# Performance work log

Measured on AMD Instinct MI355X. Metric: run time of the kernel, lower is better.

The kernel has to match this reference:

```python
import jax, jax.numpy as jnp
import numpy as np

B, T, E, U, V = 64, 100, 512, 512, 32000


def gru_layer(xs_tm, Wg, bg, Wc, bc):
    """TF GRUCell math. xs_tm: [T, B, D]. Returns (ys [T,B,U], h_final [B,U])."""
    u_dim = Wc.shape[1]
    h0 = jnp.zeros((xs_tm.shape[1], u_dim), xs_tm.dtype)

    def step(h, x):
        ru = jax.nn.sigmoid(jnp.concatenate([x, h], -1) @ Wg + bg)
        r, u = jnp.split(ru, 2, axis=-1)
        c = jnp.tanh(jnp.concatenate([x, r * h], -1) @ Wc + bc)
        h_new = u * h + (1.0 - u) * c
        return h_new, h_new

    h_final, ys = jax.lax.scan(step, h0, xs_tm)
    return ys, h_final


def setup_inputs() -> dict:
    key = jax.random.key(0)
    ks = jax.random.split(key, 16)

    def w(k, shape):
        fan_in = shape[0]
        return jax.random.normal(k, shape, jnp.float32) * (1.0 / np.sqrt(fan_in))

    inp = {
        "x": jax.random.randint(ks[0], (B, T), 0, V, jnp.int32),
        "embedding": jax.random.normal(ks[1], (V, E), jnp.float32) * 0.02,
        # bi-directional layer, input dim E
        "Wg_fw": w(ks[2], (E + U, 2 * U)), "bg_fw": jnp.ones((2 * U,), jnp.float32),
        "Wc_fw": w(ks[3], (E + U, U)),     "bc_fw": jnp.zeros((U,), jnp.float32),
        "Wg_bw": w(ks[4], (E + U, 2 * U)), "bg_bw": jnp.ones((2 * U,), jnp.float32),
        "Wc_bw": w(ks[5], (E + U, U)),     "bc_bw": jnp.zeros((U,), jnp.float32),
        # uni layer 1, input dim 2U (concat fw/bw)
        "Wg_u1": w(ks[6], (2 * U + U, 2 * U)), "bg_u1": jnp.ones((2 * U,), jnp.float32),
        "Wc_u1": w(ks[7], (2 * U + U, U)),     "bc_u1": jnp.zeros((U,), jnp.float32),
        # uni layer 2, input dim U
        "Wg_u2": w(ks[8], (U + U, 2 * U)), "bg_u2": jnp.ones((2 * U,), jnp.float32),
        "Wc_u2": w(ks[9], (U + U, U)),     "bc_u2": jnp.zeros((U,), jnp.float32),
    }
    return inp


def reference(x, embedding, Wg_fw, bg_fw, Wc_fw, bc_fw, Wg_bw, bg_bw, Wc_bw, bc_bw,
              Wg_u1, bg_u1, Wc_u1, bc_u1, Wg_u2, bg_u2, Wc_u2, bc_u2):
    emb = embedding[x]                      # [B, T, E] embedding lookup
    xs = jnp.swapaxes(emb, 0, 1)            # [T, B, E] time-major for scan
    # bidirectional GRU layer
    yf, _ = gru_layer(xs, Wg_fw, bg_fw, Wc_fw, bc_fw)
    yb, _ = gru_layer(xs[::-1], Wg_bw, bg_bw, Wc_bw, bc_bw)
    a = jnp.concatenate([yf, yb[::-1]], -1)  # [T, B, 2U]
    # 2-layer unidirectional GRU stack (MultiRNNCell)
    a, s1 = gru_layer(a, Wg_u1, bg_u1, Wc_u1, bc_u1)
    a, s2 = gru_layer(a, Wg_u2, bg_u2, Wc_u2, bc_u2)
    output = jnp.swapaxes(a, 0, 1)          # [B, T, U]
    state = jnp.stack([s1, s2])             # [2, B, U] per-layer final states
    return output, state
```

## Files before the change

### kernel.cpp

```cpp
#include <hip/hip_runtime.h>
#include <hip/hip_bf16.h>


#define TT 100

using f32x4 = __attribute__((ext_vector_type(4))) float;
using s16x8 = __attribute__((ext_vector_type(8))) short;

__device__ __forceinline__ unsigned short f2bfu(float x) {
  __hip_bfloat16 b = __float2bfloat16(x);
  unsigned short u;
  __builtin_memcpy(&u, &b, sizeof(u));
  return u;
}
__device__ __forceinline__ float bfu2f(unsigned short u) {
  __hip_bfloat16 b;
  __builtin_memcpy(&b, &u, sizeof(b));
  return __bfloat162float(b);
}
__device__ __forceinline__ float sigm(float x) {
  x = fminf(fmaxf(x, -30.f), 30.f);
  return 1.f / (1.f + __expf(-x));
}
__device__ __forceinline__ float tanh_fast(float x) {
  x = fminf(fmaxf(x, -15.f), 15.f);
  float e = __expf(-2.f * x);
  return (1.f - e) / (1.f + e);
}

__device__ __forceinline__ s16x8 sc1_load_b128(const void* p) {
  s16x8 v;
  asm volatile("global_load_dwordx4 %0, %1, off sc0 sc1" : "=v"(v) : "v"(p) : "memory");
  return v;
}
__device__ __forceinline__ void sc1_store_b16(void* p, unsigned v) {
  asm volatile("global_store_short %0, %1, off sc0 sc1" :: "v"(p), "v"(v) : "memory");
}
__device__ __forceinline__ void vm_drain() {
  asm volatile("s_waitcnt vmcnt(0)" ::: "memory");
}

__global__ __launch_bounds__(256) void pack_w_kernel(const float* __restrict__ Wg,
                                                     const float* __restrict__ Wc,
                                                     int ldg, int ldc, int ktTot,
                                                     unsigned short* __restrict__ hi,
                                                     unsigned short* __restrict__ lo) {
  const int gg = blockIdx.x * 256 + threadIdx.x;
  if (gg >= 96 * ktTot * 64) return;
  const int lane = gg & 63;
  const int pair = gg >> 6;
  const int kt = pair % ktTot;
  const int nt = pair / ktTot;
  const int kg = lane >> 4;
  const int nl = lane & 15;
  const size_t off = (size_t)gg * 8;
  for (int i = 0; i < 8; ++i) {
    const int k = kt * 32 + kg * 8 + i;
    float v = (nt < 64) ? Wg[(size_t)k * ldg + nt * 16 + nl]
                        : Wc[(size_t)k * ldc + (nt - 64) * 16 + nl];
    unsigned short h = f2bfu(v);
    hi[off + i] = h;
    lo[off + i] = f2bfu(v - bfu2f(h));
  }
}

template <int ASRC>
__global__ __launch_bounds__(256) void gemm_mfma(
    const int* __restrict__ xtok, const float* __restrict__ emb,
    const unsigned short* __restrict__ aHi, const unsigned short* __restrict__ aLo, int lda,
    const unsigned short* __restrict__ bHi, const unsigned short* __restrict__ bLo,
    int ktTot, int ktX,
    const float* __restrict__ bg, const float* __restrict__ bc,
    float* __restrict__ C) {
  __shared__ unsigned short Ah[128 * 40];
  __shared__ unsigned short Al[128 * 40];

  const int tid = threadIdx.x;
  const int lane = tid & 63;
  const int w = tid >> 6;
  const int bm = blockIdx.x, bn = blockIdx.y;
  const int fm = lane & 15, fkg = lane >> 4;

  const int arow = tid >> 1;
  const int koff = (tid & 1) * 16;
  const int rowg = bm * 128 + arow;
  int embIdx = 0;
  if (ASRC == 0) {
    const int t_ = rowg >> 6, b_ = rowg & 63;
    embIdx = xtok[b_ * TT + t_];
  }

  f32x4 acc[2][8];
#pragma unroll
  for (int rt = 0; rt < 2; ++rt)
#pragma unroll
    for (int ni = 0; ni < 8; ++ni) acc[rt][ni] = (f32x4){0.f, 0.f, 0.f, 0.f};

  for (int kt = 0; kt < ktX; ++kt) {
    __syncthreads();
    if (ASRC == 0) {
      const float* src = emb + (size_t)embIdx * 512 + kt * 32 + koff;
      s16x8 h0, h1, l0, l1;
#pragma unroll
      for (int c = 0; c < 2; ++c) {
        f32x4 va = *(const f32x4*)(src + c * 8);
        f32x4 vb = *(const f32x4*)(src + c * 8 + 4);
        s16x8 hh, ll;
#pragma unroll
        for (int j = 0; j < 4; ++j) {
          unsigned short h = f2bfu(va[j]);
          hh[j] = (short)h; ll[j] = (short)f2bfu(va[j] - bfu2f(h));
          unsigned short h2 = f2bfu(vb[j]);
          hh[j + 4] = (short)h2; ll[j + 4] = (short)f2bfu(vb[j] - bfu2f(h2));
        }
        if (c == 0) { h0 = hh; l0 = ll; } else { h1 = hh; l1 = ll; }
      }
      *(s16x8*)(Ah + arow * 40 + koff) = h0;
      *(s16x8*)(Ah + arow * 40 + koff + 8) = h1;
      *(s16x8*)(Al + arow * 40 + koff) = l0;
      *(s16x8*)(Al + arow * 40 + koff + 8) = l1;
    } else {
      const size_t so = (size_t)rowg * lda + kt * 32 + koff;
      s16x8 h0 = *(const s16x8*)(aHi + so);
      s16x8 h1 = *(const s16x8*)(aHi + so + 8);
      s16x8 l0 = *(const s16x8*)(aLo + so);
      s16x8 l1 = *(const s16x8*)(aLo + so + 8);
      *(s16x8*)(Ah + arow * 40 + koff) = h0;
      *(s16x8*)(Ah + arow * 40 + koff + 8) = h1;
      *(s16x8*)(Al + arow * 40 + koff) = l0;
      *(s16x8*)(Al + arow * 40 + koff + 8) = l1;
    }
    __syncthreads();

    s16x8 ah[2], al[2];
#pragma unroll
    for (int rt = 0; rt < 2; ++rt) {
      const int m = w * 32 + rt * 16 + fm;
      ah[rt] = *(const s16x8*)(Ah + m * 40 + fkg * 8);
      al[rt] = *(const s16x8*)(Al + m * 40 + fkg * 8);
    }
#pragma unroll
    for (int ni = 0; ni < 8; ++ni) {
      const int nt = bn * 8 + ni;
      const size_t bo = ((size_t)nt * ktTot + kt) * 512 + lane * 8;
      s16x8 bh = *(const s16x8*)(bHi + bo);
      s16x8 bl = *(const s16x8*)(bLo + bo);
#pragma unroll
      for (int rt = 0; rt < 2; ++rt) {
        acc[rt][ni] = __builtin_amdgcn_mfma_f32_16x16x32_bf16(ah[rt], bh, acc[rt][ni], 0, 0, 0);
        acc[rt][ni] = __builtin_amdgcn_mfma_f32_16x16x32_bf16(ah[rt], bl, acc[rt][ni], 0, 0, 0);
        acc[rt][ni] = __builtin_amdgcn_mfma_f32_16x16x32_bf16(al[rt], bh, acc[rt][ni], 0, 0, 0);
      }
    }
  }

#pragma unroll
  for (int ni = 0; ni < 8; ++ni) {
    const int nt = bn * 8 + ni;
    int dcol; float bias;
    if (nt < 64) { dcol = nt * 16 + fm; bias = bg[dcol]; }
    else { dcol = 1024 + (nt - 64) * 16 + fm; bias = bc[(nt - 64) * 16 + fm]; }
#pragma unroll
    for (int rt = 0; rt < 2; ++rt)
#pragma unroll
      for (int j = 0; j < 4; ++j) {
        const int row = bm * 128 + w * 32 + rt * 16 + fkg * 4 + j;
        C[(size_t)row * 1536 + dcol] = acc[rt][ni][j] + bias;
      }
  }
}

template <int NB>
__global__ __launch_bounds__(256, 1) void gru_scan_kernel(
    const float* __restrict__ gxF, const float* __restrict__ gxB,
    const unsigned short* __restrict__ wHiF, const unsigned short* __restrict__ wLoF,
    const unsigned short* __restrict__ wHiB, const unsigned short* __restrict__ wLoB,
    int ktTot, int ktH0,
    unsigned short* __restrict__ hHiG, unsigned short* __restrict__ hLoG,
    unsigned short* __restrict__ rHiG, unsigned short* __restrict__ rLoG,
    unsigned* __restrict__ slots,
    unsigned short* __restrict__ yHi, unsigned short* __restrict__ yLo, int yld,
    float* __restrict__ outb,
    float* __restrict__ stout) {
  __shared__ unsigned short wHi_s[3 * 8192];
  __shared__ unsigned short wLo_s[3 * 8192];
  __shared__ unsigned short hHi_s[8192];
  __shared__ unsigned short hLo_s[8192];
  __shared__ float scr[4][16][17];
  __shared__ float scr2[4][16][17];

  const int tid = threadIdx.x;
  const int lane = tid & 63;
  const int wv = tid >> 6;
  const int bid = blockIdx.x;
  const int g = bid & 7;
  const int wg = bid >> 3;
  const int hs = wg << 4;

  int dir = 0, b0;
  const float* gx;
  const unsigned short *wph, *wpl;
  if (NB == 16) {
    dir = g & 1;
    b0 = (g >> 1) << 4;
    gx = dir ? gxB : gxF;
    wph = dir ? wHiB : wHiF;
    wpl = dir ? wLoB : wLoF;
  } else {
    b0 = g * NB;
    gx = gxF;
    wph = wHiF;
    wpl = wLoF;
  }

  {
    const int nt0[3] = {wg, 32 + wg, 64 + wg};
    for (int c = 0; c < 3; ++c) {
      const unsigned short* sH = wph + ((size_t)nt0[c] * ktTot + ktH0) * 512;
      const unsigned short* sL = wpl + ((size_t)nt0[c] * ktTot + ktH0) * 512;
      unsigned short* dH = wHi_s + c * 8192;
      unsigned short* dL = wLo_s + c * 8192;
#pragma unroll
      for (int it = 0; it < 4; ++it) {
        const int o = (it * 256 + tid) * 8;
        *(s16x8*)(dH + o) = *(const s16x8*)(sH + o);
        *(s16x8*)(dL + o) = *(const s16x8*)(sL + o);
      }
    }
  }
  {
    s16x8 z = {0, 0, 0, 0, 0, 0, 0, 0};
#pragma unroll
    for (int it = 0; it < 4; ++it) {
      const int o = (it * 256 + tid) * 8;
      *(s16x8*)(hHi_s + o) = z;
      *(s16x8*)(hLo_s + o) = z;
    }
  }
  __syncthreads();

  unsigned* gslots = slots + g * 32;

  const int fm = lane & 15;
  const int fkg = lane >> 4;
  const int arow = fm * 512;
  const int asw = (fm & 7) << 3;
  const int akof = fkg * 8;

  const int ob = tid >> 4, oj = tid & 15;
  const bool own = (ob < NB);
  const int ui = ob * 512 + ((hs + oj) ^ ((ob & 7) << 3));

  const size_t tileo = (size_t)g * 8192;

  auto mfma_tile = [&](int cidx, float (*dst)[16][17]) {
    f32x4 acc0 = {0.f, 0.f, 0.f, 0.f}, acc1 = {0.f, 0.f, 0.f, 0.f};
    const int ktb = wv * 4;
#pragma unroll
    for (int q = 0; q < 4; ++q) {
      const int kt = ktb + q;
      const int ao = arow + ((kt * 32 + akof) ^ asw);
      s16x8 ah = *(const s16x8*)(hHi_s + ao);
      s16x8 al = *(const s16x8*)(hLo_s + ao);
      const int wo = ((cidx * 16 + kt) * 64 + lane) * 8;
      s16x8 bh = *(const s16x8*)(wHi_s + wo);
      s16x8 bl = *(const s16x8*)(wLo_s + wo);
      if (q & 1) {
        acc1 = __builtin_amdgcn_mfma_f32_16x16x32_bf16(ah, bh, acc1, 0, 0, 0);
        acc1 = __builtin_amdgcn_mfma_f32_16x16x32_bf16(ah, bl, acc1, 0, 0, 0);
        acc1 = __builtin_amdgcn_mfma_f32_16x16x32_bf16(al, bh, acc1, 0, 0, 0);
      } else {
        acc0 = __builtin_amdgcn_mfma_f32_16x16x32_bf16(ah, bh, acc0, 0, 0, 0);
        acc0 = __builtin_amdgcn_mfma_f32_16x16x32_bf16(ah, bl, acc0, 0, 0, 0);
        acc0 = __builtin_amdgcn_mfma_f32_16x16x32_bf16(al, bh, acc0, 0, 0, 0);
      }
    }
#pragma unroll
    for (int j = 0; j < 4; ++j) dst[wv][fkg * 4 + j][fm] = acc0[j] + acc1[j];
  };

  auto load_tile = [&](const unsigned short* SH, const unsigned short* SL) {
    s16x8 th[NB / 4], tl[NB / 4];
#pragma unroll
    for (int it = 0; it < NB / 4; ++it) {
      const int o = (it * 256 + tid) * 8;
      th[it] = sc1_load_b128(SH + tileo + o);
      tl[it] = sc1_load_b128(SL + tileo + o);
    }
    vm_drain();
#pragma unroll
    for (int it = 0; it < NB / 4; ++it) {
      const int o = (it * 256 + tid) * 8;
      *(s16x8*)(hHi_s + o) = th[it];
      *(s16x8*)(hLo_s + o) = tl[it];
    }
  };

  auto poll = [&](unsigned target) {
    if (tid < 32) {
      const unsigned* p = gslots + tid;
      unsigned v;
      do {
        asm volatile("global_load_dword %0, %1, off sc0 sc1\n\ts_waitcnt vmcnt(0)"
                     : "=v"(v) : "v"(p) : "memory");
      } while (!__all(v >= target));
    }
    __syncthreads();
  };

  float gxr = 0.f, gxu = 0.f, gxc = 0.f;
  if (own) {
    const float* row = gx + ((size_t)(dir ? TT - 1 : 0) * 64 + b0 + ob) * 1536 + hs + oj;
    gxr = row[0]; gxu = row[512]; gxc = row[1024];
  }

  for (int t = 0; t < TT; ++t) {
    const int tg = dir ? (TT - 1 - t) : t;

    mfma_tile(0, scr);
    __syncthreads();

    float hv = 0.f;
    if (own) {
      float rpre = scr[0][ob][oj] + scr[1][ob][oj] + scr[2][ob][oj] + scr[3][ob][oj] + gxr;
      float sg = sigm(rpre);
      hv = bfu2f(hHi_s[ui]) + bfu2f(hLo_s[ui]);
      float rh = sg * hv;
      unsigned short rhh = f2bfu(rh);
      sc1_store_b16(rHiG + tileo + ui, rhh);
      sc1_store_b16(rLoG + tileo + ui, f2bfu(rh - bfu2f(rhh)));
    }
    vm_drain();
    __syncthreads();
    if (tid == 0) {
      unsigned* p = gslots + wg;
      unsigned tv = 2 * t + 1;
      asm volatile("global_store_dword %0, %1, off sc0 sc1" :: "v"(p), "v"(tv) : "memory");
    }

    mfma_tile(1, scr2);

    float ngxr = 0.f, ngxu = 0.f, ngxc = 0.f;
    if (own && t + 1 < TT) {
      const int tgn = dir ? (TT - 2 - t) : (t + 1);
      const float* row = gx + ((size_t)tgn * 64 + b0 + ob) * 1536 + hs + oj;
      ngxr = row[0]; ngxu = row[512]; ngxc = row[1024];
    }

    poll(2 * t + 1);
    load_tile(rHiG, rLoG);
    __syncthreads();

    mfma_tile(2, scr);
    __syncthreads();

    float hn = 0.f;
    unsigned short hh_ = 0, ll_ = 0;
    if (own) {
      float upre = scr2[0][ob][oj] + scr2[1][ob][oj] + scr2[2][ob][oj] + scr2[3][ob][oj] + gxu;
      float uv = sigm(upre);
      float cpre = scr[0][ob][oj] + scr[1][ob][oj] + scr[2][ob][oj] + scr[3][ob][oj] + gxc;
      float cv = tanh_fast(cpre);
      hn = uv * hv + (1.f - uv) * cv;
      hh_ = f2bfu(hn);
      ll_ = f2bfu(hn - bfu2f(hh_));
    }

    if (t == TT - 1) {
      if (own) {
        if (yHi) {
          const int ycol = (NB == 16) ? (dir * 512 + hs + oj) : (hs + oj);
          const size_t yi = ((size_t)tg * 64 + (b0 + ob)) * yld + ycol;
          yHi[yi] = hh_; yLo[yi] = ll_;
        }
        if (outb) outb[((size_t)(b0 + ob) * TT + t) * 512 + hs + oj] = hn;
        if (stout) stout[(size_t)(b0 + ob) * 512 + hs + oj] = hn;
      }
      break;
    }

    if (own) {
      sc1_store_b16(hHiG + tileo + ui, hh_);
      sc1_store_b16(hLoG + tileo + ui, ll_);
    }
    vm_drain();
    __syncthreads();
    if (tid == 0) {
      unsigned* p = gslots + wg;
      unsigned tv = 2 * t + 2;
      asm volatile("global_store_dword %0, %1, off sc0 sc1" :: "v"(p), "v"(tv) : "memory");
    }

    if (own) {
      if (yHi) {
        const int ycol = (NB == 16) ? (dir * 512 + hs + oj) : (hs + oj);
        const size_t yi = ((size_t)tg * 64 + (b0 + ob)) * yld + ycol;
        yHi[yi] = hh_; yLo[yi] = ll_;
      }
      if (outb) outb[((size_t)(b0 + ob) * TT + t) * 512 + hs + oj] = hn;
    }
    gxr = ngxr; gxu = ngxu; gxc = ngxc;

    poll(2 * t + 2);
    load_tile(hHiG, hLoG);
    __syncthreads();
  }
}

extern "C" void kernel_launch(void* const* d_in, const int* in_sizes, int n_in,
                              void* d_out, int out_size, void* d_ws, size_t ws_size,
                              hipStream_t stream) {
  (void)in_sizes; (void)n_in; (void)out_size; (void)ws_size;
  const int* x = (const int*)d_in[0];
  const float* emb = (const float*)d_in[1];
  const float* WgFw = (const float*)d_in[2];
  const float* bgFw = (const float*)d_in[3];
  const float* WcFw = (const float*)d_in[4];
  const float* bcFw = (const float*)d_in[5];
  const float* WgBw = (const float*)d_in[6];
  const float* bgBw = (const float*)d_in[7];
  const float* WcBw = (const float*)d_in[8];
  const float* bcBw = (const float*)d_in[9];
  const float* WgU1 = (const float*)d_in[10];
  const float* bgU1 = (const float*)d_in[11];
  const float* WcU1 = (const float*)d_in[12];
  const float* bcU1 = (const float*)d_in[13];
  const float* WgU2 = (const float*)d_in[14];
  const float* bgU2 = (const float*)d_in[15];
  const float* WcU2 = (const float*)d_in[16];
  const float* bcU2 = (const float*)d_in[17];

  char* ws = (char*)d_ws;
  float* bufA = (float*)(ws + 0);
  float* bufB = (float*)(ws + 39321600);
  unsigned short* ycatHi = (unsigned short*)(ws + 78643200);
  unsigned short* ycatLo = (unsigned short*)(ws + 91750400);
  unsigned short* y1Hi = (unsigned short*)(ws + 78643200);
  unsigned short* y1Lo = (unsigned short*)(ws + 85196800);
  unsigned short* wpFwHi = (unsigned short*)(ws + 104857600);
  unsigned short* wpFwLo = (unsigned short*)(ws + 108003328);
  unsigned short* wpBwHi = (unsigned short*)(ws + 111149056);
  unsigned short* wpBwLo = (unsigned short*)(ws + 114294784);
  unsigned short* wpU1Hi = (unsigned short*)(ws + 117440512);
  unsigned short* wpU1Lo = (unsigned short*)(ws + 122159104);
  unsigned short* wpU2Hi = (unsigned short*)(ws + 117440512);
  unsigned short* wpU2Lo = (unsigned short*)(ws + 120586240);
  unsigned short* hb = (unsigned short*)(ws + 126877696);
  unsigned* bars = (unsigned*)(ws + 127401984);

  unsigned short* hHiG = hb;
  unsigned short* hLoG = hb + 65536;
  unsigned short* rHiG = hb + 131072;
  unsigned short* rLoG = hb + 196608;

  float* out = (float*)d_out;
  float* st1 = out + (size_t)64 * TT * 512;
  float* st2 = st1 + 64 * 512;

  hipMemsetAsync(bars, 0, 4096, stream);

  pack_w_kernel<<<768, 256, 0, stream>>>(WgFw, WcFw, 1024, 512, 32, wpFwHi, wpFwLo);
  pack_w_kernel<<<768, 256, 0, stream>>>(WgBw, WcBw, 1024, 512, 32, wpBwHi, wpBwLo);
  pack_w_kernel<<<1152, 256, 0, stream>>>(WgU1, WcU1, 1024, 512, 48, wpU1Hi, wpU1Lo);

  gemm_mfma<0><<<dim3(50, 12), 256, 0, stream>>>(
      x, emb, nullptr, nullptr, 0, wpFwHi, wpFwLo, 32, 16, bgFw, bcFw, bufA);
  gemm_mfma<0><<<dim3(50, 12), 256, 0, stream>>>(
      x, emb, nullptr, nullptr, 0, wpBwHi, wpBwLo, 32, 16, bgBw, bcBw, bufB);

  {
    const float *a0 = bufA, *a1 = bufB;
    const unsigned short *w0 = wpFwHi, *w1 = wpFwLo, *w2 = wpBwHi, *w3 = wpBwLo;
    int ktT = 32, ktH = 16;
    unsigned short *h0 = hHiG, *h1 = hLoG, *r0 = rHiG, *r1 = rLoG;
    unsigned* bp = bars;
    unsigned short *yh = ycatHi, *yl = ycatLo; int yld = 1024;
    float *on = nullptr, *sn = nullptr;
    void* args[] = {&a0, &a1, &w0, &w1, &w2, &w3, &ktT, &ktH, &h0, &h1, &r0, &r1,
                    &bp, &yh, &yl, &yld, &on, &sn};
    hipLaunchCooperativeKernel((const void*)gru_scan_kernel<16>, dim3(256), dim3(256),
                               args, 0, stream);
  }

  gemm_mfma<1><<<dim3(50, 12), 256, 0, stream>>>(
      nullptr, nullptr, ycatHi, ycatLo, 1024, wpU1Hi, wpU1Lo, 48, 32, bgU1, bcU1, bufA);

  {
    const float *a0 = bufA, *a1 = nullptr;
    const unsigned short *w0 = wpU1Hi, *w1 = wpU1Lo, *w2 = nullptr, *w3 = nullptr;
    int ktT = 48, ktH = 32;
    unsigned short *h0 = hHiG, *h1 = hLoG, *r0 = rHiG, *r1 = rLoG;
    unsigned* bp = bars + 256;
    unsigned short *yh = y1Hi, *yl = y1Lo; int yld = 512;
    float *on = nullptr, *sn = st1;
    void* args[] = {&a0, &a1, &w0, &w1, &w2, &w3, &ktT, &ktH, &h0, &h1, &r0, &r1,
                    &bp, &yh, &yl, &yld, &on, &sn};
    hipLaunchCooperativeKernel((const void*)gru_scan_kernel<8>, dim3(256), dim3(256),
                               args, 0, stream);
  }

  pack_w_kernel<<<768, 256, 0, stream>>>(WgU2, WcU2, 1024, 512, 32, wpU2Hi, wpU2Lo);

  gemm_mfma<1><<<dim3(50, 12), 256, 0, stream>>>(
      nullptr, nullptr, y1Hi, y1Lo, 512, wpU2Hi, wpU2Lo, 32, 16, bgU2, bcU2, bufB);

  {
    const float *a0 = bufB, *a1 = nullptr;
    const unsigned short *w0 = wpU2Hi, *w1 = wpU2Lo, *w2 = nullptr, *w3 = nullptr;
    int ktT = 32, ktH = 16;
    unsigned short *h0 = hHiG, *h1 = hLoG, *r0 = rHiG, *r1 = rLoG;
    unsigned* bp = bars + 512;
    unsigned short *yh = nullptr, *yl = nullptr; int yld = 0;
    float *on = out, *sn = st2;
    void* args[] = {&a0, &a1, &w0, &w1, &w2, &w3, &ktT, &ktH, &h0, &h1, &r0, &r1,
                    &bp, &yh, &yl, &yld, &on, &sn};
    hipLaunchCooperativeKernel((const void*)gru_scan_kernel<8>, dim3(256), dim3(256),
                               args, 0, stream);
  }
}
```

Baseline: 1.783 ms.

## Load packed hidden-state fragments straight from global into registers, skipping LDS staging

The hi/lo bf16 halves of the shared hidden and reset-gated state now live interleaved in one 32-bit word in global memory. Each wave loads its MFMA A-fragments directly from global (bypassing cache) into registers and unpacks them with bit operations, instead of copying the whole tile into shared memory and paying an extra barrier. The per-step h fragments are loaded once and reused for both gate and candidate matmuls, and the global state buffer is zeroed with a memset before each scan. This is meant to cut LDS round-trips and a __syncthreads per half-step on the serial recurrence path. The cost is more global load traffic per wave and some ALU work to unpack.

```diff
diff --git a/kernel.cpp b/kernel.cpp
--- a/kernel.cpp
+++ b/kernel.cpp
@@ -6,6 +6,7 @@
 
 using f32x4 = __attribute__((ext_vector_type(4))) float;
 using s16x8 = __attribute__((ext_vector_type(8))) short;
+using u32x4 = __attribute__((ext_vector_type(4))) unsigned;
 
 __device__ __forceinline__ unsigned short f2bfu(float x) {
   __hip_bfloat16 b = __float2bfloat16(x);
@@ -26,15 +27,6 @@
   x = fminf(fmaxf(x, -15.f), 15.f);
   float e = __expf(-2.f * x);
   return (1.f - e) / (1.f + e);
-}
-
-__device__ __forceinline__ s16x8 sc1_load_b128(const void* p) {
-  s16x8 v;
-  asm volatile("global_load_dwordx4 %0, %1, off sc0 sc1" : "=v"(v) : "v"(p) : "memory");
-  return v;
-}
-__device__ __forceinline__ void sc1_store_b16(void* p, unsigned v) {
-  asm volatile("global_store_short %0, %1, off sc0 sc1" :: "v"(p), "v"(v) : "memory");
 }
 __device__ __forceinline__ void vm_drain() {
   asm volatile("s_waitcnt vmcnt(0)" ::: "memory");
@@ -176,16 +168,13 @@
     const unsigned short* __restrict__ wHiF, const unsigned short* __restrict__ wLoF,
     const unsigned short* __restrict__ wHiB, const unsigned short* __restrict__ wLoB,
     int ktTot, int ktH0,
-    unsigned short* __restrict__ hHiG, unsigned short* __restrict__ hLoG,
-    unsigned short* __restrict__ rHiG, unsigned short* __restrict__ rLoG,
+    unsigned* __restrict__ hPkG, unsigned* __restrict__ rPkG,
     unsigned* __restrict__ slots,
     unsigned short* __restrict__ yHi, unsigned short* __restrict__ yLo, int yld,
     float* __restrict__ outb,
     float* __restrict__ stout) {
   __shared__ unsigned short wHi_s[3 * 8192];
   __shared__ unsigned short wLo_s[3 * 8192];
-  __shared__ unsigned short hHi_s[8192];
-  __shared__ unsigned short hLo_s[8192];
   __shared__ float scr[4][16][17];
   __shared__ float scr2[4][16][17];
 
@@ -228,24 +217,14 @@
       }
     }
   }
-  {
-    s16x8 z = {0, 0, 0, 0, 0, 0, 0, 0};
-#pragma unroll
-    for (int it = 0; it < 4; ++it) {
-      const int o = (it * 256 + tid) * 8;
-      *(s16x8*)(hHi_s + o) = z;
-      *(s16x8*)(hLo_s + o) = z;
-    }
-  }
   __syncthreads();
 
   unsigned* gslots = slots + g * 32;
 
   const int fm = lane & 15;
   const int fkg = lane >> 4;
-  const int arow = fm * 512;
+  const int afe = fm * 512;
   const int asw = (fm & 7) << 3;
-  const int akof = fkg * 8;
 
   const int ob = tid >> 4, oj = tid & 15;
   const bool own = (ob < NB);
@@ -253,46 +232,59 @@
 
   const size_t tileo = (size_t)g * 8192;
 
-  auto mfma_tile = [&](int cidx, float (*dst)[16][17]) {
+  auto mfma_regs = [&](int cidx, const s16x8* ah, const s16x8* al,
+                       float (*dst)[16][17]) {
     f32x4 acc0 = {0.f, 0.f, 0.f, 0.f}, acc1 = {0.f, 0.f, 0.f, 0.f};
-    const int ktb = wv * 4;
 #pragma unroll
     for (int q = 0; q < 4; ++q) {
-      const int kt = ktb + q;
-      const int ao = arow + ((kt * 32 + akof) ^ asw);
-      s16x8 ah = *(const s16x8*)(hHi_s + ao);
-      s16x8 al = *(const s16x8*)(hLo_s + ao);
+      const int kt = wv * 4 + q;
       const int wo = ((cidx * 16 + kt) * 64 + lane) * 8;
       s16x8 bh = *(const s16x8*)(wHi_s + wo);
       s16x8 bl = *(const s16x8*)(wLo_s + wo);
       if (q & 1) {
-        acc1 = __builtin_amdgcn_mfma_f32_16x16x32_bf16(ah, bh, acc1, 0, 0, 0);
-        acc1 = __builtin_amdgcn_mfma_f32_16x16x32_bf16(ah, bl, acc1, 0, 0, 0);
-        acc1 = __builtin_amdgcn_mfma_f32_16x16x32_bf16(al, bh, acc1, 0, 0, 0);
+        acc1 = __builtin_amdgcn_mfma_f32_16x16x32_bf16(ah[q], bh, acc1, 0, 0, 0);
+        acc1 = __builtin_amdgcn_mfma_f32_16x16x32_bf16(ah[q], bl, acc1, 0, 0, 0);
+        acc1 = __builtin_amdgcn_mfma_f32_16x16x32_bf16(al[q], bh, acc1, 0, 0, 0);
       } else {
-        acc0 = __builtin_amdgcn_mfma_f32_16x16x32_bf16(ah, bh, acc0, 0, 0, 0);
-        acc0 = __builtin_amdgcn_mfma_f32_16x16x32_bf16(ah, bl, acc0, 0, 0, 0);
-        acc0 = __builtin_amdgcn_mfma_f32_16x16x32_bf16(al, bh, acc0, 0, 0, 0);
+        acc0 = __builtin_amdgcn_mfma_f32_16x16x32_bf16(ah[q], bh, acc0, 0, 0, 0);
+        acc0 = __builtin_amdgcn_mfma_f32_16x16x32_bf16(ah[q], bl, acc0, 0, 0, 0);
+        acc0 = __builtin_amdgcn_mfma_f32_16x16x32_bf16(al[q], bh, acc0, 0, 0, 0);
       }
     }
 #pragma unroll
     for (int j = 0; j < 4; ++j) dst[wv][fkg * 4 + j][fm] = acc0[j] + acc1[j];
   };
 
-  auto load_tile = [&](const unsigned short* SH, const unsigned short* SL) {
-    s16x8 th[NB / 4], tl[NB / 4];
-#pragma unroll
-    for (int it = 0; it < NB / 4; ++it) {
-      const int o = (it * 256 + tid) * 8;
-      th[it] = sc1_load_b128(SH + tileo + o);
-      tl[it] = sc1_load_b128(SL + tileo + o);
-    }
+  auto load_frags = [&](const unsigned* pk, s16x8* ah, s16x8* al,
+                        bool withHv, unsigned* hvOut) {
+    u32x4 d[4][2];
+#pragma unroll
+    for (int q = 0; q < 4; ++q) {
+      const int kt = wv * 4 + q;
+      const unsigned* p = pk + tileo + afe + ((kt * 32 + fkg * 8) ^ asw);
+      asm volatile("global_load_dwordx4 %0, %1, off sc0 sc1"
+                   : "=v"(d[q][0]) : "v"(p) : "memory");
+      asm volatile("global_load_dwordx4 %0, %1, off sc0 sc1"
+                   : "=v"(d[q][1]) : "v"(p + 4) : "memory");
+    }
+    if (withHv && own)
+      asm volatile("global_load_dword %0, %1, off sc0 sc1"
+                   : "=v"(*hvOut) : "v"(pk + tileo + ui) : "memory");
     vm_drain();
-#pragma unroll
-    for (int it = 0; it < NB / 4; ++it) {
-      const int o = (it * 256 + tid) * 8;
-      *(s16x8*)(hHi_s + o) = th[it];
-      *(s16x8*)(hLo_s + o) = tl[it];
+    __builtin_amdgcn_sched_barrier(0);
+#pragma unroll
+    for (int q = 0; q < 4; ++q) {
+      u32x4 hh, ll;
+#pragma unroll
+      for (int i = 0; i < 2; ++i) {
+        const u32x4 dd = d[q][i];
+        hh[2 * i] = (dd[0] & 0xffffu) | (dd[1] << 16);
+        hh[2 * i + 1] = (dd[2] & 0xffffu) | (dd[3] << 16);
+        ll[2 * i] = (dd[0] >> 16) | (dd[1] & 0xffff0000u);
+        ll[2 * i + 1] = (dd[2] >> 16) | (dd[3] & 0xffff0000u);
+      }
+      __builtin_memcpy(&ah[q], &hh, 16);
+      __builtin_memcpy(&al[q], &ll, 16);
     }
   };
 
@@ -317,28 +309,33 @@
   for (int t = 0; t < TT; ++t) {
     const int tg = dir ? (TT - 1 - t) : t;
 
-    mfma_tile(0, scr);
+    s16x8 ah[4], al[4];
+    unsigned hvu = 0;
+    load_frags(hPkG, ah, al, true, &hvu);
+    mfma_regs(0, ah, al, scr);
     __syncthreads();
 
     float hv = 0.f;
     if (own) {
       float rpre = scr[0][ob][oj] + scr[1][ob][oj] + scr[2][ob][oj] + scr[3][ob][oj] + gxr;
       float sg = sigm(rpre);
-      hv = bfu2f(hHi_s[ui]) + bfu2f(hLo_s[ui]);
+      hv = bfu2f((unsigned short)(hvu & 0xffffu)) + bfu2f((unsigned short)(hvu >> 16));
       float rh = sg * hv;
-      unsigned short rhh = f2bfu(rh);
-      sc1_store_b16(rHiG + tileo + ui, rhh);
-      sc1_store_b16(rLoG + tileo + ui, f2bfu(rh - bfu2f(rhh)));
+      unsigned short hh_ = f2bfu(rh);
+      unsigned short ll_ = f2bfu(rh - bfu2f(hh_));
+      unsigned e = (unsigned)hh_ | ((unsigned)ll_ << 16);
+      asm volatile("global_store_dword %0, %1, off sc0 sc1"
+                   :: "v"(rPkG + tileo + ui), "v"(e) : "memory");
     }
     vm_drain();
     __syncthreads();
     if (tid == 0) {
-      unsigned* p = gslots + wg;
       unsigned tv = 2 * t + 1;
-      asm volatile("global_store_dword %0, %1, off sc0 sc1" :: "v"(p), "v"(tv) : "memory");
-    }
-
-    mfma_tile(1, scr2);
+      asm volatile("global_store_dword %0, %1, off sc0 sc1"
+                   :: "v"(gslots + wg), "v"(tv) : "memory");
+    }
+
+    mfma_regs(1, ah, al, scr2);
 
     float ngxr = 0.f, ngxu = 0.f, ngxc = 0.f;
     if (own && t + 1 < TT) {
@@ -348,10 +345,9 @@
     }
 
     poll(2 * t + 1);
-    load_tile(rHiG, rLoG);
-    __syncthreads();
-
-    mfma_tile(2, scr);
+
+    load_frags(rPkG, ah, al, false, nullptr);
+    mfma_regs(2, ah, al, scr);
     __syncthreads();
 
     float hn = 0.f;
@@ -380,15 +376,16 @@
     }
 
     if (own) {
-      sc1_store_b16(hHiG + tileo + ui, hh_);
-      sc1_store_b16(hLoG + tileo + ui, ll_);
+      unsigned e = (unsigned)hh_ | ((unsigned)ll_ << 16);
+      asm volatile("global_store_dword %0, %1, off sc0 sc1"
+                   :: "v"(hPkG + tileo + ui), "v"(e) : "memory");
     }
     vm_drain();
     __syncthreads();
     if (tid == 0) {
-      unsigned* p = gslots + wg;
       unsigned tv = 2 * t + 2;
-      asm volatile("global_store_dword %0, %1, off sc0 sc1" :: "v"(p), "v"(tv) : "memory");
+      asm volatile("global_store_dword %0, %1, off sc0 sc1"
+                   :: "v"(gslots + wg), "v"(tv) : "memory");
     }
 
     if (own) {
@@ -402,8 +399,6 @@
     gxr = ngxr; gxu = ngxu; gxc = ngxc;
 
     poll(2 * t + 2);
-    load_tile(hHiG, hLoG);
-    __syncthreads();
   }
 }
 
@@ -445,13 +440,9 @@
   unsigned short* wpU1Lo = (unsigned short*)(ws + 122159104);
   unsigned short* wpU2Hi = (unsigned short*)(ws + 117440512);
   unsigned short* wpU2Lo = (unsigned short*)(ws + 120586240);
-  unsigned short* hb = (unsigned short*)(ws + 126877696);
+  unsigned* hPkG = (unsigned*)(ws + 126877696);
+  unsigned* rPkG = (unsigned*)(ws + 127139840);
   unsigned* bars = (unsigned*)(ws + 127401984);
-
-  unsigned short* hHiG = hb;
-  unsigned short* hLoG = hb + 65536;
-  unsigned short* rHiG = hb + 131072;
-  unsigned short* rLoG = hb + 196608;
 
   float* out = (float*)d_out;
   float* st1 = out + (size_t)64 * TT * 512;
@@ -468,15 +459,16 @@
   gemm_mfma<0><<<dim3(50, 12), 256, 0, stream>>>(
       x, emb, nullptr, nullptr, 0, wpBwHi, wpBwLo, 32, 16, bgBw, bcBw, bufB);
 
+  hipMemsetAsync(hPkG, 0, 524288, stream);
   {
     const float *a0 = bufA, *a1 = bufB;
     const unsigned short *w0 = wpFwHi, *w1 = wpFwLo, *w2 = wpBwHi, *w3 = wpBwLo;
     int ktT = 32, ktH = 16;
-    unsigned short *h0 = hHiG, *h1 = hLoG, *r0 = rHiG, *r1 = rLoG;
+    unsigned *h0 = hPkG, *r0 = rPkG;
     unsigned* bp = bars;
     unsigned short *yh = ycatHi, *yl = ycatLo; int yld = 1024;
     float *on = nullptr, *sn = nullptr;
-    void* args[] = {&a0, &a1, &w0, &w1, &w2, &w3, &ktT, &ktH, &h0, &h1, &r0, &r1,
+    void* args[] = {&a0, &a1, &w0, &w1, &w2, &w3, &ktT, &ktH, &h0, &r0,
                     &bp, &yh, &yl, &yld, &on, &sn};
     hipLaunchCooperativeKernel((const void*)gru_scan_kernel<16>, dim3(256), dim3(256),
                                args, 0, stream);
@@ -485,15 +477,16 @@
   gemm_mfma<1><<<dim3(50, 12), 256, 0, stream>>>(
       nullptr, nullptr, ycatHi, ycatLo, 1024, wpU1Hi, wpU1Lo, 48, 32, bgU1, bcU1, bufA);
 
+  hipMemsetAsync(hPkG, 0, 524288, stream);
   {
     const float *a0 = bufA, *a1 = nullptr;
     const unsigned short *w0 = wpU1Hi, *w1 = wpU1Lo, *w2 = nullptr, *w3 = nullptr;
     int ktT = 48, ktH = 32;
-    unsigned short *h0 = hHiG, *h1 = hLoG, *r0 = rHiG, *r1 = rLoG;
+    unsigned *h0 = hPkG, *r0 = rPkG;
     unsigned* bp = bars + 256;
     unsigned short *yh = y1Hi, *yl = y1Lo; int yld = 512;
     float *on = nullptr, *sn = st1;
-    void* args[] = {&a0, &a1, &w0, &w1, &w2, &w3, &ktT, &ktH, &h0, &h1, &r0, &r1,
+    void* args[] = {&a0, &a1, &w0, &w1, &w2, &w3, &ktT, &ktH, &h0, &r0,
                     &bp, &yh, &yl, &yld, &on, &sn};
     hipLaunchCooperativeKernel((const void*)gru_scan_kernel<8>, dim3(256), dim3(256),
                                args, 0, stream);
@@ -504,15 +497,16 @@
   gemm_mfma<1><<<dim3(50, 12), 256, 0, stream>>>(
       nullptr, nullptr, y1Hi, y1Lo, 512, wpU2Hi, wpU2Lo, 32, 16, bgU2, bcU2, bufB);
 
+  hipMemsetAsync(hPkG, 0, 524288, stream);
   {
     const float *a0 = bufB, *a1 = nullptr;
     const unsigned short *w0 = wpU2Hi, *w1 = wpU2Lo, *w2 = nullptr, *w3 = nullptr;
     int ktT = 32, ktH = 16;
-    unsigned short *h0 = hHiG, *h1 = hLoG, *r0 = rHiG, *r1 = rLoG;
+    unsigned *h0 = hPkG, *r0 = rPkG;
     unsigned* bp = bars + 512;
     unsigned short *yh = nullptr, *yl = nullptr; int yld = 0;
     float *on = out, *sn = st2;
-    void* args[] = {&a0, &a1, &w0, &w1, &w2, &w3, &ktT, &ktH, &h0, &h1, &r0, &r1,
+    void* args[] = {&a0, &a1, &w0, &w1, &w2, &w3, &ktT, &ktH, &h0, &r0,
                     &bp, &yh, &yl, &yld, &on, &sn};
     hipLaunchCooperativeKernel((const void*)gru_scan_kernel<8>, dim3(256), dim3(256),
                                args, 0, stream);
```

Result: no change. 1.810 ms (+1.5%).
